# Kernel tuning notes

Hardware: AMD Instinct MI355X
Metric: run time of the kernel (lower is better)

Reference implementation:

```python
import jax, jax.numpy as jnp
import numpy as np
from jax import lax

THD = 0.8  # Lowe ratio-test threshold (module init kwarg `thd`)


def setup_inputs() -> dict:
    key = jax.random.key(0)
    k1, k2 = jax.random.split(key)
    desc1 = jax.random.normal(k1, (16384, 128), dtype=jnp.float32)
    desc2 = jax.random.normal(k2, (16384, 128), dtype=jnp.float32)
    return {"desc1": desc1, "desc2": desc2}


def _cdist(a, b):
    # Euclidean pairwise distances, (B1, B2), same math as torch.cdist(p=2)
    sq_a = jnp.sum(a * a, axis=-1, keepdims=True)          # (B1, 1)
    sq_b = jnp.sum(b * b, axis=-1)                          # (B2,)
    d2 = sq_a + sq_b - 2.0 * (a @ b.T)                      # (B1, B2)
    return jnp.sqrt(jnp.maximum(d2, 0.0))


def reference(desc1, desc2):
    cost = _cdist(desc1, desc2)                             # (B1, B2)
    # two smallest distances per row
    neg_vals, idxs_in_2 = lax.top_k(-cost, 2)               # (B1, 2) each
    vals = -neg_vals
    ratio = vals[:, 0] / vals[:, 1]                         # (B1,)
    mask = ratio <= THD                                     # (B1,) bool
    # jit-compatible padded outputs: masked-out rows carry 0 distance; the
    # boolean mask selects the valid (idxs_in1, idxs_in2) match rows, which is
    # the compaction torch does with boolean indexing.
    match_dists = jnp.where(mask, ratio, 0.0)               # (B1,)
    idxs_in1 = jnp.arange(desc1.shape[0], dtype=jnp.int32)
    matches_idxs = jnp.stack([idxs_in1, idxs_in_2[:, 0].astype(jnp.int32)], axis=1)  # (B1, 2)
    return match_dists, matches_idxs, mask
```

## Files before the change

### kernel.cpp

```cpp
#include <hip/hip_runtime.h>
#include <math.h>
#include <float.h>
#include <stdint.h>


typedef __attribute__((ext_vector_type(4))) float     f32x4;
typedef __attribute__((ext_vector_type(8))) _Float16  half8;

#define D_     128
#define BM_    64
#define BN_    128
#define CS_    2
#define PARTS_ 4

__device__ __forceinline__ void gload_lds16(const void* g, void* l) {
  auto gp = (const __attribute__((address_space(1))) unsigned int*)(uintptr_t)g;
  auto lp = (__attribute__((address_space(3))) unsigned int*)(uintptr_t)l;
  __builtin_amdgcn_global_load_lds(gp, lp, 16, 0, 0);
}

__global__ void norms_kernel(const float* __restrict__ d1,
                             const float* __restrict__ d2,
                             float* __restrict__ sq, int B) {
  int gid  = blockIdx.x * blockDim.x + threadIdx.x;
  int wid  = gid >> 6;
  int lane = gid & 63;
  if (wid >= 2 * B) return;
  const float* src = (wid < B) ? (d1 + (size_t)wid * D_)
                               : (d2 + (size_t)(wid - B) * D_);
  float2 v = ((const float2*)src)[lane];
  float s = fmaf(v.x, v.x, v.y * v.y);
  #pragma unroll
  for (int off = 32; off > 0; off >>= 1) s += __shfl_down(s, off, 64);
  if (lane == 0) sq[wid] = s;
}

__global__ void convert_kernel(const float* __restrict__ d1, const float* __restrict__ d2,
                               _Float16* __restrict__ Ahi, _Float16* __restrict__ Alo,
                               _Float16* __restrict__ BhiP, _Float16* __restrict__ BloP,
                               int B) {
  int i = blockIdx.x * blockDim.x + threadIdx.x;
  int total = B * 16;
  if (i >= 2 * total) return;
  bool isB = i >= total;
  int j    = isB ? i - total : i;
  int desc = j >> 4;
  int seg  = j & 15;
  const float* src = (isB ? d2 : d1) + (size_t)desc * D_ + seg * 8;
  float4 v0 = *(const float4*)(src);
  float4 v1 = *(const float4*)(src + 4);
  half8 hv, lv;
  float e[8] = {v0.x, v0.y, v0.z, v0.w, v1.x, v1.y, v1.z, v1.w};
  #pragma unroll
  for (int q = 0; q < 8; ++q) {
    _Float16 h = (_Float16)e[q];
    hv[q] = h;
    lv[q] = (_Float16)(e[q] - (float)h);
  }
  if (!isB) {
    *(half8*)(Ahi + (size_t)desc * D_ + seg * 8) = hv;
    *(half8*)(Alo + (size_t)desc * D_ + seg * 8) = lv;
  } else {
    int t   = desc >> 7, cloc = desc & 127;
    int nf  = cloc >> 4, c15  = cloc & 15;
    int kk  = seg >> 2,  gq   = seg & 3;
    size_t off = (size_t)t * 16384 + kk * 4096 + nf * 512 + gq * 128 + c15 * 8;
    *(half8*)(BhiP + off) = hv;
    *(half8*)(BloP + off) = lv;
  }
}

__global__ __launch_bounds__(256, 2)
void nn_mfma(const _Float16* __restrict__ Ahi, const _Float16* __restrict__ Alo,
             const _Float16* __restrict__ BhiP, const _Float16* __restrict__ BloP,
             const float* __restrict__ sqb,
             float* __restrict__ p_d0, float* __restrict__ p_d1,
             int* __restrict__ p_j0, int B) {
  extern __shared__ char smem[];
  const int tid  = threadIdx.x;
  const int lane = tid & 63;
  const int wid  = tid >> 6;
  const int wr   = wid >> 1;
  const int wc   = wid & 1;
  const int l15  = lane & 15;
  const int g    = lane >> 4;

  const int nrb   = B / BM_;
  const int rb    = blockIdx.x % nrb;
  const int cspl  = blockIdx.x / nrb;
  const int i0    = rb * BM_;
  const int niter = (B / CS_) / BN_;
  const int tile0 = cspl * niter;

  half8 ah[2][4], al[2][4];
  #pragma unroll
  for (int mf = 0; mf < 2; ++mf) {
    int row = i0 + wr * 32 + mf * 16 + l15;
    const _Float16* pa = Ahi + (size_t)row * D_ + g * 8;
    const _Float16* pl = Alo + (size_t)row * D_ + g * 8;
    #pragma unroll
    for (int kk = 0; kk < 4; ++kk) {
      ah[mf][kk] = *(const half8*)(pa + kk * 32);
      al[mf][kk] = *(const half8*)(pl + kk * 32);
    }
  }

  const _Float16* srcH = BhiP + (size_t)tile0 * 16384 + wid * 4096 + lane * 8;
  const _Float16* srcL = BloP + (size_t)tile0 * 16384 + wid * 4096 + lane * 8;
  char* ldsH = smem + wid * 8192;
  char* ldsL = smem + 32768 + wid * 8192;

  const int rdbase = lane * 16 + wc * 4096;
  const int colg0  = tile0 * BN_ + wc * 64 + l15;

  float best0[8], best1[8]; int bj[8];
  #pragma unroll
  for (int s = 0; s < 8; ++s) { best0[s] = FLT_MAX; best1[s] = FLT_MAX; bj[s] = 0x7fffffff; }

  for (int it = 0; it < niter; ++it) {
    __syncthreads();
    #pragma unroll
    for (int e = 0; e < 8; ++e) gload_lds16(srcH + e * 512, ldsH + e * 1024);
    #pragma unroll
    for (int e = 0; e < 8; ++e) gload_lds16(srcL + e * 512, ldsL + e * 1024);
    srcH += 16384;
    srcL += 16384;
    __syncthreads();

    f32x4 acc[2][4];
    #pragma unroll
    for (int mf = 0; mf < 2; ++mf)
      #pragma unroll
      for (int nf = 0; nf < 4; ++nf) acc[mf][nf] = (f32x4){0.f, 0.f, 0.f, 0.f};

    #pragma unroll
    for (int kk = 0; kk < 4; ++kk) {
      half8 bh[4], bl[4];
      #pragma unroll
      for (int nf = 0; nf < 4; ++nf) {
        bh[nf] = *(const half8*)(smem + rdbase + kk * 8192 + nf * 1024);
        bl[nf] = *(const half8*)(smem + rdbase + kk * 8192 + nf * 1024 + 32768);
      }
      #pragma unroll
      for (int mf = 0; mf < 2; ++mf)
        #pragma unroll
        for (int nf = 0; nf < 4; ++nf) {
          acc[mf][nf] = __builtin_amdgcn_mfma_f32_16x16x32_f16(ah[mf][kk], bh[nf], acc[mf][nf], 0, 0, 0);
          acc[mf][nf] = __builtin_amdgcn_mfma_f32_16x16x32_f16(ah[mf][kk], bl[nf], acc[mf][nf], 0, 0, 0);
          acc[mf][nf] = __builtin_amdgcn_mfma_f32_16x16x32_f16(al[mf][kk], bh[nf], acc[mf][nf], 0, 0, 0);
        }
    }

    #pragma unroll
    for (int nf = 0; nf < 4; ++nf) {
      int colg = colg0 + it * BN_ + nf * 16;
      float sj = sqb[colg];
      #pragma unroll
      for (int mf = 0; mf < 2; ++mf)
        #pragma unroll
        for (int r = 0; r < 4; ++r) {
          int s = mf * 4 + r;
          float t = fmaf(-2.f, acc[mf][nf][r], sj);
          bool lt0 = t < best0[s];
          best1[s] = fminf(best1[s], fmaxf(t, best0[s]));
          best0[s] = fminf(t, best0[s]);
          bj[s]    = lt0 ? colg : bj[s];
        }
    }
  }

  #pragma unroll
  for (int off = 1; off < 16; off <<= 1) {
    #pragma unroll
    for (int s = 0; s < 8; ++s) {
      float e0 = __shfl_xor(best0[s], off, 64);
      float e1 = __shfl_xor(best1[s], off, 64);
      int   f0 = __shfl_xor(bj[s],    off, 64);
      if (e0 < best0[s] || (e0 == best0[s] && f0 < bj[s])) {
        best1[s] = fminf(best0[s], e1);
        best0[s] = e0;
        bj[s]    = f0;
      } else {
        best1[s] = fminf(best1[s], e0);
      }
    }
  }

  if (l15 == 0) {
    int part = cspl * 2 + wc;
    #pragma unroll
    for (int s = 0; s < 8; ++s) {
      int mf = s >> 2, r = s & 3;
      int row = i0 + wr * 32 + mf * 16 + g * 4 + r;
      p_d0[row * PARTS_ + part] = best0[s];
      p_d1[row * PARTS_ + part] = best1[s];
      p_j0[row * PARTS_ + part] = bj[s];
    }
  }
}

__global__ void nn_final(const float* __restrict__ sqa,
                         const float* __restrict__ p_d0,
                         const float* __restrict__ p_d1,
                         const int* __restrict__ p_j0,
                         float* __restrict__ out, int B) {
  int row = blockIdx.x * blockDim.x + threadIdx.x;
  if (row >= B) return;
  float d0 = FLT_MAX, d1 = FLT_MAX;
  int j0 = 0x7fffffff;
  for (int cs = 0; cs < PARTS_; ++cs) {
    float e0 = p_d0[row * PARTS_ + cs];
    float e1 = p_d1[row * PARTS_ + cs];
    int   f0 = p_j0[row * PARTS_ + cs];
    if (e0 < d0 || (e0 == d0 && f0 < j0)) {
      d1 = fminf(d0, e1);
      d0 = e0;
      j0 = f0;
    } else {
      d1 = fminf(d1, e0);
    }
  }
  float sa = sqa[row];
  float v0 = sqrtf(fmaxf(sa + d0, 0.f));
  float v1 = sqrtf(fmaxf(sa + d1, 0.f));
  float ratio = v0 / v1;
  bool m = (ratio <= 0.8f);
  out[row]             = m ? ratio : 0.f;
  out[B + row * 2]     = (float)row;
  out[B + row * 2 + 1] = (float)j0;
  out[3 * B + row]     = m ? 1.f : 0.f;
}

extern "C" void kernel_launch(void* const* d_in, const int* in_sizes, int n_in,
                              void* d_out, int out_size, void* d_ws, size_t ws_size,
                              hipStream_t stream) {
  const float* d1 = (const float*)d_in[0];
  const float* d2 = (const float*)d_in[1];
  const int B = in_sizes[0] / D_;

  float* ws   = (float*)d_ws;
  float* sqa  = ws;
  float* sqb  = ws + B;
  float* p_d0 = ws + 2 * B;
  float* p_d1 = ws + 6 * B;
  int*   p_j0 = (int*)(ws + 10 * B);
  _Float16* Ahi  = (_Float16*)(ws + 14 * B);
  _Float16* Alo  = Ahi + (size_t)B * D_;
  _Float16* BhiP = Alo + (size_t)B * D_;
  _Float16* BloP = BhiP + (size_t)B * D_;

  int nthreads = 2 * B * 64;
  norms_kernel<<<(nthreads + 255) / 256, 256, 0, stream>>>(d1, d2, sqa, B);

  int ngroups = 2 * B * 16;
  convert_kernel<<<(ngroups + 255) / 256, 256, 0, stream>>>(d1, d2, Ahi, Alo, BhiP, BloP, B);

  hipFuncSetAttribute((const void*)nn_mfma,
                      hipFuncAttributeMaxDynamicSharedMemorySize, 65536);
  nn_mfma<<<(B / BM_) * CS_, 256, 65536, stream>>>(Ahi, Alo, BhiP, BloP, sqb,
                                                   p_d0, p_d1, p_j0, B);

  nn_final<<<(B + 255) / 256, 256, 0, stream>>>(sqa, p_d0, p_d1, p_j0, (float*)d_out, B);
}
```

Baseline: 208.9 us.

## Double-buffer B tiles in LDS, fold norms and -2 scale into MFMA

The distance kernel now stages each B tile into one of two LDS buffers while computing on the other, replacing the two-barrier load-then-compute loop with a software pipeline. The tile shape changes to 128 rows by 64 columns, with each wave owning 32 rows and all 64 columns, and the column split goes from 2 to 4. The -2 factor is baked into the packed B halves during conversion, and the column norm seeds the MFMA accumulator, so the epilogue fma and per-iteration norm load disappear. Risks: an fp16 -2 scale of the lo part can lose subnormal precision, and the unrolled-by-two loop assumes an even iteration count.

```diff
diff --git a/kernel.cpp b/kernel.cpp
--- a/kernel.cpp
+++ b/kernel.cpp
@@ -8,9 +8,9 @@
 typedef __attribute__((ext_vector_type(8))) _Float16  half8;
 
 #define D_     128
-#define BM_    64
-#define BN_    128
-#define CS_    2
+#define BM_    128
+#define BN_    64
+#define CS_    4
 #define PARTS_ 4
 
 __device__ __forceinline__ void gload_lds16(const void* g, void* l) {
@@ -54,17 +54,18 @@
   #pragma unroll
   for (int q = 0; q < 8; ++q) {
     _Float16 h = (_Float16)e[q];
-    hv[q] = h;
-    lv[q] = (_Float16)(e[q] - (float)h);
+    _Float16 l = (_Float16)(e[q] - (float)h);
+    if (isB) { h = (_Float16)(-2.0f) * h; l = (_Float16)(-2.0f) * l; }
+    hv[q] = h; lv[q] = l;
   }
   if (!isB) {
     *(half8*)(Ahi + (size_t)desc * D_ + seg * 8) = hv;
     *(half8*)(Alo + (size_t)desc * D_ + seg * 8) = lv;
   } else {
-    int t   = desc >> 7, cloc = desc & 127;
+    int t   = desc >> 6, cloc = desc & 63;
     int nf  = cloc >> 4, c15  = cloc & 15;
     int kk  = seg >> 2,  gq   = seg & 3;
-    size_t off = (size_t)t * 16384 + kk * 4096 + nf * 512 + gq * 128 + c15 * 8;
+    size_t off = (size_t)t * 8192 + kk * 2048 + nf * 512 + gq * 128 + c15 * 8;
     *(half8*)(BhiP + off) = hv;
     *(half8*)(BloP + off) = lv;
   }
@@ -80,8 +81,6 @@
   const int tid  = threadIdx.x;
   const int lane = tid & 63;
   const int wid  = tid >> 6;
-  const int wr   = wid >> 1;
-  const int wc   = wid & 1;
   const int l15  = lane & 15;
   const int g    = lane >> 4;
 
@@ -95,7 +94,7 @@
   half8 ah[2][4], al[2][4];
   #pragma unroll
   for (int mf = 0; mf < 2; ++mf) {
-    int row = i0 + wr * 32 + mf * 16 + l15;
+    int row = i0 + wid * 32 + mf * 16 + l15;
     const _Float16* pa = Ahi + (size_t)row * D_ + g * 8;
     const _Float16* pl = Alo + (size_t)row * D_ + g * 8;
     #pragma unroll
@@ -105,47 +104,58 @@
     }
   }
 
-  const _Float16* srcH = BhiP + (size_t)tile0 * 16384 + wid * 4096 + lane * 8;
-  const _Float16* srcL = BloP + (size_t)tile0 * 16384 + wid * 4096 + lane * 8;
-  char* ldsH = smem + wid * 8192;
-  char* ldsL = smem + 32768 + wid * 8192;
-
-  const int rdbase = lane * 16 + wc * 4096;
-  const int colg0  = tile0 * BN_ + wc * 64 + l15;
+  const _Float16* srcH0 = BhiP + (size_t)tile0 * 8192 + wid * 2048 + lane * 8;
+  const _Float16* srcL0 = BloP + (size_t)tile0 * 8192 + wid * 2048 + lane * 8;
+  char* ldsHW = smem + wid * 4096;
+  auto stage = [&](int bufbase, int it) {
+    const _Float16* sH = srcH0 + (size_t)it * 8192;
+    const _Float16* sL = srcL0 + (size_t)it * 8192;
+    char* lH = ldsHW + bufbase;
+    char* lL = ldsHW + bufbase + 16384;
+    #pragma unroll
+    for (int e = 0; e < 4; ++e) gload_lds16(sH + e * 512, lH + e * 1024);
+    #pragma unroll
+    for (int e = 0; e < 4; ++e) gload_lds16(sL + e * 512, lL + e * 1024);
+  };
 
   float best0[8], best1[8]; int bj[8];
   #pragma unroll
   for (int s = 0; s < 8; ++s) { best0[s] = FLT_MAX; best1[s] = FLT_MAX; bj[s] = 0x7fffffff; }
 
-  for (int it = 0; it < niter; ++it) {
-    __syncthreads();
-    #pragma unroll
-    for (int e = 0; e < 8; ++e) gload_lds16(srcH + e * 512, ldsH + e * 1024);
-    #pragma unroll
-    for (int e = 0; e < 8; ++e) gload_lds16(srcL + e * 512, ldsL + e * 1024);
-    srcH += 16384;
-    srcL += 16384;
-    __syncthreads();
+  float sjA[4], sjB[4];
+  const int colg0 = tile0 * BN_ + l15;
+
+  stage(0, 0);
+  #pragma unroll
+  for (int nf = 0; nf < 4; ++nf) sjA[nf] = sqb[colg0 + nf * 16];
+  __syncthreads();
+
+  auto body = [&](int it, int bufbase, float (&sjc)[4], float (&sjn)[4]) {
+    if (it + 1 < niter) {
+      stage(bufbase ^ 32768, it + 1);
+      #pragma unroll
+      for (int nf = 0; nf < 4; ++nf) sjn[nf] = sqb[colg0 + (it + 1) * BN_ + nf * 16];
+    }
 
     f32x4 acc[2][4];
-    #pragma unroll
-    for (int mf = 0; mf < 2; ++mf)
-      #pragma unroll
-      for (int nf = 0; nf < 4; ++nf) acc[mf][nf] = (f32x4){0.f, 0.f, 0.f, 0.f};
-
     #pragma unroll
     for (int kk = 0; kk < 4; ++kk) {
       half8 bh[4], bl[4];
       #pragma unroll
       for (int nf = 0; nf < 4; ++nf) {
-        bh[nf] = *(const half8*)(smem + rdbase + kk * 8192 + nf * 1024);
-        bl[nf] = *(const half8*)(smem + rdbase + kk * 8192 + nf * 1024 + 32768);
+        bh[nf] = *(const half8*)(smem + bufbase + kk * 4096 + nf * 1024 + lane * 16);
+        bl[nf] = *(const half8*)(smem + bufbase + 16384 + kk * 4096 + nf * 1024 + lane * 16);
       }
       #pragma unroll
       for (int mf = 0; mf < 2; ++mf)
         #pragma unroll
         for (int nf = 0; nf < 4; ++nf) {
-          acc[mf][nf] = __builtin_amdgcn_mfma_f32_16x16x32_f16(ah[mf][kk], bh[nf], acc[mf][nf], 0, 0, 0);
+          if (kk == 0) {
+            f32x4 c0 = {sjc[nf], sjc[nf], sjc[nf], sjc[nf]};
+            acc[mf][nf] = __builtin_amdgcn_mfma_f32_16x16x32_f16(ah[mf][0], bh[nf], c0, 0, 0, 0);
+          } else {
+            acc[mf][nf] = __builtin_amdgcn_mfma_f32_16x16x32_f16(ah[mf][kk], bh[nf], acc[mf][nf], 0, 0, 0);
+          }
           acc[mf][nf] = __builtin_amdgcn_mfma_f32_16x16x32_f16(ah[mf][kk], bl[nf], acc[mf][nf], 0, 0, 0);
           acc[mf][nf] = __builtin_amdgcn_mfma_f32_16x16x32_f16(al[mf][kk], bh[nf], acc[mf][nf], 0, 0, 0);
         }
@@ -154,19 +164,24 @@
     #pragma unroll
     for (int nf = 0; nf < 4; ++nf) {
       int colg = colg0 + it * BN_ + nf * 16;
-      float sj = sqb[colg];
       #pragma unroll
       for (int mf = 0; mf < 2; ++mf)
         #pragma unroll
         for (int r = 0; r < 4; ++r) {
           int s = mf * 4 + r;
-          float t = fmaf(-2.f, acc[mf][nf][r], sj);
+          float t = acc[mf][nf][r];
           bool lt0 = t < best0[s];
           best1[s] = fminf(best1[s], fmaxf(t, best0[s]));
           best0[s] = fminf(t, best0[s]);
           bj[s]    = lt0 ? colg : bj[s];
         }
     }
+    __syncthreads();
+  };
+
+  for (int itp = 0; itp < niter; itp += 2) {
+    body(itp,     0,     sjA, sjB);
+    body(itp + 1, 32768, sjB, sjA);
   }
 
   #pragma unroll
@@ -187,14 +202,13 @@
   }
 
   if (l15 == 0) {
-    int part = cspl * 2 + wc;
     #pragma unroll
     for (int s = 0; s < 8; ++s) {
       int mf = s >> 2, r = s & 3;
-      int row = i0 + wr * 32 + mf * 16 + g * 4 + r;
-      p_d0[row * PARTS_ + part] = best0[s];
-      p_d1[row * PARTS_ + part] = best1[s];
-      p_j0[row * PARTS_ + part] = bj[s];
+      int row = i0 + wid * 32 + mf * 16 + g * 4 + r;
+      p_d0[row * PARTS_ + cspl] = best0[s];
+      p_d1[row * PARTS_ + cspl] = best1[s];
+      p_j0[row * PARTS_ + cspl] = bj[s];
     }
   }
 }
```

New measurement: 194.5 us. 6.9% less time.
